# Kernel tuning notes

Hardware: AMD Instinct MI355X
Metric: run time of the kernel (lower is better)

## Reference

```python
import jax, jax.numpy as jnp
import numpy as np

N_NODES = 50000
N_EDGES = 800000
IN_C = 256
HID_C = 256
OUT_C = 128
N_GRAPHS = 256


def setup_inputs() -> dict:
    key = jax.random.key(0)
    ks = jax.random.split(key, 12)
    x = jax.random.normal(ks[0], (N_NODES, IN_C), dtype=jnp.float32)
    src = jax.random.randint(ks[1], (N_EDGES,), 0, N_NODES, dtype=jnp.int32)
    dst = jnp.sort(jax.random.randint(ks[2], (N_EDGES,), 0, N_NODES, dtype=jnp.int32))
    p = jax.random.uniform(ks[3], (N_NODES,), dtype=jnp.float32)
    batch = jnp.sort(jax.random.randint(ks[4], (N_NODES,), 0, N_GRAPHS, dtype=jnp.int32))
    root_ptr = jax.random.randint(ks[5], (N_GRAPHS,), 0, N_NODES, dtype=jnp.int32)
    s1 = 1.0 / np.sqrt(IN_C)
    s2 = 1.0 / np.sqrt(HID_C)
    s3 = 1.0 / np.sqrt(2 * HID_C)
    Wl1 = jax.random.uniform(ks[6], (IN_C, HID_C), jnp.float32, -s1, s1)
    Wr1 = jax.random.uniform(ks[7], (IN_C, HID_C), jnp.float32, -s1, s1)
    b1 = jnp.zeros((HID_C,), jnp.float32)
    Wl2 = jax.random.uniform(ks[8], (HID_C, HID_C), jnp.float32, -s2, s2)
    Wr2 = jax.random.uniform(ks[9], (HID_C, HID_C), jnp.float32, -s2, s2)
    b2 = jnp.zeros((HID_C,), jnp.float32)
    Wlin = jax.random.uniform(ks[10], (2 * HID_C, OUT_C), jnp.float32, -s3, s3)
    blin = jax.random.uniform(ks[11], (OUT_C,), jnp.float32, -s3, s3)
    return {"x": x, "src": src, "dst": dst, "p": p, "batch": batch,
            "root_ptr": root_ptr, "num_graphs": N_GRAPHS,
            "Wl1": Wl1, "Wr1": Wr1, "b1": b1,
            "Wl2": Wl2, "Wr2": Wr2, "b2": b2,
            "Wlin": Wlin, "blin": blin}


def _sage_conv(x, src, dst, inv_deg, Wl, Wr, b):
    # mean aggregation of neighbor features: scatter-add then divide by degree
    agg = jax.ops.segment_sum(x[src], dst, num_segments=N_NODES)  # [N, d]
    agg = agg * inv_deg[:, None]
    return agg @ Wl + x @ Wr + b


def reference(x, src, dst, p, batch, root_ptr, num_graphs,
              Wl1, Wr1, b1, Wl2, Wr2, b2, Wlin, blin):
    # in-degree for mean aggregation (shared by both convs)
    deg = jax.ops.segment_sum(jnp.ones_like(dst, dtype=x.dtype), dst,
                              num_segments=N_NODES)
    inv_deg = jnp.where(deg > 0, 1.0 / jnp.maximum(deg, 1.0), 0.0)

    h = _sage_conv(x, src, dst, inv_deg, Wl1, Wr1, b1)
    h = jax.nn.relu(h)  # dropout is identity in eval mode
    h = _sage_conv(h, src, dst, inv_deg, Wl2, Wr2, b2)

    # masked mean pool of p-weighted features per graph
    pw = h * p[:, None]
    gsum = jax.ops.segment_sum(pw, batch, num_segments=num_graphs)
    gcnt = jax.ops.segment_sum(jnp.ones_like(p), batch, num_segments=num_graphs)
    gmean = gsum / jnp.maximum(gcnt, 1.0)[:, None]

    feat = jnp.concatenate([h[root_ptr], gmean], axis=-1)  # [G, 2*hid]
    return feat @ Wlin + blin
```

## Files before the change

kernel.cpp:

```cpp
#include <hip/hip_runtime.h>
#include <hip/hip_bf16.h>

#define N_NODES 50000
#define N_EDGES 800000
#define C_DIM   256
#define OUT_C   128
#define N_GRAPHS 256

typedef unsigned short ushort8 __attribute__((ext_vector_type(8)));
typedef __bf16         bf16x8  __attribute__((ext_vector_type(8)));
typedef float          f32x4   __attribute__((ext_vector_type(4)));

typedef __attribute__((address_space(1))) const unsigned int gu32;
typedef __attribute__((address_space(3))) unsigned int lu32;

#if __has_builtin(__builtin_amdgcn_sched_barrier)
#define SCHED_FENCE() __builtin_amdgcn_sched_barrier(0)
#else
#define SCHED_FENCE() ((void)0)
#endif

__device__ __forceinline__ float us2f(unsigned short u) {
    unsigned int x = ((unsigned int)u) << 16;
    return __builtin_bit_cast(float, x);
}
__device__ __forceinline__ unsigned short f2bf(float f) {
    unsigned int u = __builtin_bit_cast(unsigned int, f);
    u += 0x7fffu + ((u >> 16) & 1u);
    return (unsigned short)(u >> 16);
}

__device__ __forceinline__ int lower_bound_i(const int* __restrict__ a, int n, int v) {
    int lo = 0, hi = n;
    while (lo < hi) {
        int mid = (lo + hi) >> 1;
        if (a[mid] < v) lo = mid + 1; else hi = mid;
    }
    return lo;
}

__global__ void preprocess(const float* __restrict__ x, unsigned short* __restrict__ xb,
                           const float* __restrict__ W0, const float* __restrict__ W1,
                           const float* __restrict__ W2, const float* __restrict__ W3,
                           unsigned short* __restrict__ D0, unsigned short* __restrict__ D1,
                           unsigned short* __restrict__ D2, unsigned short* __restrict__ D3,
                           const int* __restrict__ dst, const int* __restrict__ batch,
                           int* __restrict__ row_ptr, int* __restrict__ graph_ptr,
                           float* __restrict__ inv_deg) {
    int b = blockIdx.x;
    int t = threadIdx.x;
    if (b < 12500) {
        int i = b * 256 + t;
        float4 v = *(const float4*)(x + ((size_t)i << 2));
        ushort4 o;
        o.x = f2bf(v.x); o.y = f2bf(v.y); o.z = f2bf(v.z); o.w = f2bf(v.w);
        *(ushort4*)(xb + ((size_t)i << 2)) = o;
    } else if (b < 13524) {
        int sub = b - 12500;
        const float* S; unsigned short* D;
        switch (sub >> 8) {
            case 0: S = W0; D = D0; break;
            case 1: S = W1; D = D1; break;
            case 2: S = W2; D = D2; break;
            default: S = W3; D = D3; break;
        }
        int i = (sub & 255) * 256 + t;
        int k = i >> 8, n = i & 255;
        D[n * 256 + k] = f2bf(S[i]);
    } else {
        int i = (b - 13524) * 256 + t;
        if (i <= N_NODES) {
            int lb = lower_bound_i(dst, N_EDGES, i);
            row_ptr[i] = lb;
            if (i < N_NODES) {
                int ub = lower_bound_i(dst, N_EDGES, i + 1);
                int cnt = ub - lb;
                inv_deg[i] = (cnt > 0) ? (1.0f / (float)cnt) : 0.0f;
            }
        }
        if (i <= N_GRAPHS) graph_ptr[i] = lower_bound_i(batch, N_NODES, i);
    }
}

__global__ void aggregate(const unsigned short* __restrict__ X,
                          const int* __restrict__ src,
                          const int* __restrict__ row_ptr,
                          const float* __restrict__ inv_deg,
                          unsigned short* __restrict__ out) {
    int gw   = (blockIdx.x * blockDim.x + threadIdx.x) >> 6;
    int lane = threadIdx.x & 63;
    if (gw >= N_NODES) return;
    int e0 = row_ptr[gw], e1 = row_ptr[gw + 1];
    const int lo = lane << 2;
    float a0 = 0.f, a1 = 0.f, a2 = 0.f, a3 = 0.f;
    int e = e0;

    for (; e + 16 <= e1; e += 16) {
        ushort4 v[16];
#pragma unroll
        for (int j = 0; j < 16; ++j) {
            int s = __builtin_amdgcn_readfirstlane(src[e + j]);
            v[j] = *(const ushort4*)(X + ((size_t)s << 8) + lo);
        }
        SCHED_FENCE();
#pragma unroll
        for (int j = 0; j < 16; ++j) {
            a0 += us2f(v[j].x); a1 += us2f(v[j].y);
            a2 += us2f(v[j].z); a3 += us2f(v[j].w);
        }
    }
    int rem = e1 - e;
    if (rem > 0) {
        int cl = e1 - 1;
        ushort4 v[16]; float w[16];
#pragma unroll
        for (int j = 0; j < 16; ++j) {
            int ej = e + j;
            int ec = ej < cl ? ej : cl;
            w[j] = (ej < e1) ? 1.0f : 0.0f;
            int s = __builtin_amdgcn_readfirstlane(src[ec]);
            v[j] = *(const ushort4*)(X + ((size_t)s << 8) + lo);
        }
        SCHED_FENCE();
#pragma unroll
        for (int j = 0; j < 16; ++j) {
            a0 = fmaf(us2f(v[j].x), w[j], a0);
            a1 = fmaf(us2f(v[j].y), w[j], a1);
            a2 = fmaf(us2f(v[j].z), w[j], a2);
            a3 = fmaf(us2f(v[j].w), w[j], a3);
        }
    }

    float sc = inv_deg[gw];
    ushort4 o;
    o.x = f2bf(a0 * sc); o.y = f2bf(a1 * sc); o.z = f2bf(a2 * sc); o.w = f2bf(a3 * sc);
    *(ushort4*)(out + ((size_t)gw << 8) + lo) = o;
}

__global__ __launch_bounds__(256, 3)
void gemm_fused(const unsigned short* __restrict__ A1,
                const unsigned short* __restrict__ A2,
                const unsigned short* __restrict__ B1t,
                const unsigned short* __restrict__ B2t,
                const float* __restrict__ bias,
                unsigned short* __restrict__ C,
                int M, int do_relu) {
    __shared__ __align__(16) unsigned short As[4096];
    __shared__ __align__(16) unsigned short Bs[16384];

    const int t    = threadIdx.x;
    const int m0   = blockIdx.x * 64;
    const int lane = t & 63, wid = t >> 6;
    const int wn   = wid * 64;
    const int lrow = lane & 15;
    const int kq   = lane >> 4;

    const f32x4 zero4 = {0.f, 0.f, 0.f, 0.f};
    f32x4 acc[4][4];
#pragma unroll
    for (int i = 0; i < 4; ++i)
#pragma unroll
        for (int j = 0; j < 4; ++j) acc[i][j] = zero4;

    for (int it = 0; it < 8; ++it) {
        const unsigned short* __restrict__ Ab = (it < 4) ? A1 : A2;
        const unsigned short* __restrict__ Bb = (it < 4) ? B1t : B2t;
        int ko = (it * 64) & 255;

#pragma unroll
        for (int i = 0; i < 2; ++i) {
            int q   = t + i * 256;
            int row = q >> 3;
            int kb  = (q & 7) ^ (row & 7);
            const unsigned short* ga = Ab + (size_t)(m0 + row) * 256 + ko + kb * 8;
            __builtin_amdgcn_global_load_lds((gu32*)ga, (lu32*)(As + q * 8), 16, 0, 0);
        }
#pragma unroll
        for (int i = 0; i < 8; ++i) {
            int q   = t + i * 256;
            int row = q >> 3;
            int kb  = (q & 7) ^ (row & 7);
            const unsigned short* gb = Bb + (size_t)row * 256 + ko + kb * 8;
            __builtin_amdgcn_global_load_lds((gu32*)gb, (lu32*)(Bs + q * 8), 16, 0, 0);
        }
        __syncthreads();

#pragma unroll
        for (int s = 0; s < 2; ++s) {
            int kqp = s * 4 + kq;
            bf16x8 af[4], bfr[4];
#pragma unroll
            for (int mi = 0; mi < 4; ++mi) {
                int r = mi * 16 + lrow;
                int slot = r * 8 + (kqp ^ (lrow & 7));
                uint4 u = *(const uint4*)(As + slot * 8);
                af[mi] = __builtin_bit_cast(bf16x8, u);
            }
#pragma unroll
            for (int ni = 0; ni < 4; ++ni) {
                int r = wn + ni * 16 + lrow;
                int slot = r * 8 + (kqp ^ (lrow & 7));
                uint4 u = *(const uint4*)(Bs + slot * 8);
                bfr[ni] = __builtin_bit_cast(bf16x8, u);
            }
#pragma unroll
            for (int mi = 0; mi < 4; ++mi)
#pragma unroll
                for (int ni = 0; ni < 4; ++ni)
                    acc[mi][ni] = __builtin_amdgcn_mfma_f32_16x16x32_bf16(
                        af[mi], bfr[ni], acc[mi][ni], 0, 0, 0);
        }
        __syncthreads();
    }

    const int rbase = (lane >> 4) * 4;
#pragma unroll
    for (int ni = 0; ni < 4; ++ni) {
        int n  = wn + ni * 16 + lrow;
        float bv = bias[n];
#pragma unroll
        for (int mi = 0; mi < 4; ++mi) {
            int mb = m0 + mi * 16 + rbase;
#pragma unroll
            for (int r = 0; r < 4; ++r) {
                int m = mb + r;
                if (m < M) {
                    float v = acc[mi][ni][r] + bv;
                    if (do_relu) v = fmaxf(v, 0.f);
                    C[(size_t)m * 256 + n] = f2bf(v);
                }
            }
        }
    }
}

__global__ void pool_final(const unsigned short* __restrict__ h2,
                           const float* __restrict__ p,
                           const int* __restrict__ graph_ptr,
                           const int* __restrict__ root_ptr,
                           const float* __restrict__ Wlin,
                           const float* __restrict__ blin,
                           float* __restrict__ out) {
    __shared__ float fl[512];
    int g = blockIdx.x;
    int c = threadIdx.x;
    int s = graph_ptr[g], e = graph_ptr[g + 1];
    float acc = 0.f;
    for (int n = s; n < e; n += 8) {
        int cl = e - 1;
        float w[8]; unsigned short v[8];
#pragma unroll
        for (int j = 0; j < 8; ++j) {
            int nj = n + j;
            int ncj = nj < cl ? nj : cl;
            int nu = __builtin_amdgcn_readfirstlane(ncj);
            w[j] = (nj < e) ? p[nu] : 0.0f;
            v[j] = h2[(size_t)nu * 256 + c];
        }
        SCHED_FENCE();
#pragma unroll
        for (int j = 0; j < 8; ++j)
            acc = fmaf(us2f(v[j]), w[j], acc);
    }
    float cnt = (float)(e - s);
    int root = root_ptr[g];
    fl[c]       = us2f(h2[(size_t)root * 256 + c]);
    fl[256 + c] = acc / fmaxf(cnt, 1.0f);
    __syncthreads();

    int o = threadIdx.x;
    if (o < 128) {
        float s0 = 0.f, s1 = 0.f, s2 = 0.f, s3 = 0.f;
        for (int k = 0; k < 512; k += 4) {
            s0 = fmaf(fl[k + 0], Wlin[(k + 0) * 128 + o], s0);
            s1 = fmaf(fl[k + 1], Wlin[(k + 1) * 128 + o], s1);
            s2 = fmaf(fl[k + 2], Wlin[(k + 2) * 128 + o], s2);
            s3 = fmaf(fl[k + 3], Wlin[(k + 3) * 128 + o], s3);
        }
        out[(size_t)g * 128 + o] = blin[o] + ((s0 + s1) + (s2 + s3));
    }
}

extern "C" void kernel_launch(void* const* d_in, const int* in_sizes, int n_in,
                              void* d_out, int out_size, void* d_ws, size_t ws_size,
                              hipStream_t stream) {
    const float* x        = (const float*)d_in[0];
    const int*   src      = (const int*)d_in[1];
    const int*   dst      = (const int*)d_in[2];
    const float* p        = (const float*)d_in[3];
    const int*   batch    = (const int*)d_in[4];
    const int*   root_ptr = (const int*)d_in[5];
    const float* Wl1  = (const float*)d_in[7];
    const float* Wr1  = (const float*)d_in[8];
    const float* b1   = (const float*)d_in[9];
    const float* Wl2  = (const float*)d_in[10];
    const float* Wr2  = (const float*)d_in[11];
    const float* b2   = (const float*)d_in[12];
    const float* Wlin = (const float*)d_in[13];
    const float* blin = (const float*)d_in[14];
    float* out = (float*)d_out;

    size_t off = 0;
    char* base = (char*)d_ws;
    auto alloc = [&](size_t bytes) -> void* {
        void* q = base + off;
        off += (bytes + 255) & ~(size_t)255;
        return q;
    };
    int*            row_ptr   = (int*)  alloc((N_NODES + 1) * sizeof(int));
    int*            graph_ptr = (int*)  alloc((N_GRAPHS + 1) * sizeof(int));
    float*          inv_deg   = (float*)alloc(N_NODES * sizeof(float));
    unsigned short* Wl1t = (unsigned short*)alloc(256 * 256 * 2);
    unsigned short* Wr1t = (unsigned short*)alloc(256 * 256 * 2);
    unsigned short* Wl2t = (unsigned short*)alloc(256 * 256 * 2);
    unsigned short* Wr2t = (unsigned short*)alloc(256 * 256 * 2);
    unsigned short* xb   = (unsigned short*)alloc((size_t)N_NODES * 256 * 2);
    unsigned short* aggb = (unsigned short*)alloc((size_t)N_NODES * 256 * 2);
    unsigned short* h1   = (unsigned short*)alloc((size_t)N_NODES * 256 * 2);
    unsigned short* h2   = (unsigned short*)alloc((size_t)N_NODES * 256 * 2);
    (void)ws_size; (void)n_in; (void)in_sizes; (void)out_size;

    preprocess<<<13720, 256, 0, stream>>>(x, xb, Wl1, Wr1, Wl2, Wr2,
                                          Wl1t, Wr1t, Wl2t, Wr2t,
                                          dst, batch, row_ptr, graph_ptr, inv_deg);

    dim3 ggrid((N_NODES + 63) / 64);

    aggregate<<<N_NODES / 4, 256, 0, stream>>>(xb, src, row_ptr, inv_deg, aggb);
    gemm_fused<<<ggrid, 256, 0, stream>>>(aggb, xb, Wl1t, Wr1t, b1, h1, N_NODES, 1);

    aggregate<<<N_NODES / 4, 256, 0, stream>>>(h1, src, row_ptr, inv_deg, aggb);
    gemm_fused<<<ggrid, 256, 0, stream>>>(aggb, h1, Wl2t, Wr2t, b2, h2, N_NODES, 0);

    pool_final<<<N_GRAPHS, 256, 0, stream>>>(h2, p, graph_ptr, root_ptr,
                                             Wlin, blin, out);
}
```

Before: 345.2 us.

## Fuse neighbor aggregation into SAGE conv GEMM via LDS-resident tile

Merges the mean-aggregation gather and the dual GEMM into one kernel per layer: each block gathers 64 rows of neighbor means into a swizzled LDS tile, then runs MFMA against it and the self features. This removes the global write and reread of the aggregated buffer and one launch per layer. B weights and self-features are now read directly from global memory per fragment instead of staged through LDS, and gather parallelism per block is reduced, which risks worse latency hiding.

New measurement: 386.4 us. +11.9%, slower.

```diff
diff --git a/kernel.cpp b/kernel.cpp
--- a/kernel.cpp
+++ b/kernel.cpp
@@ -10,9 +10,6 @@
 typedef unsigned short ushort8 __attribute__((ext_vector_type(8)));
 typedef __bf16         bf16x8  __attribute__((ext_vector_type(8)));
 typedef float          f32x4   __attribute__((ext_vector_type(4)));
-
-typedef __attribute__((address_space(1))) const unsigned int gu32;
-typedef __attribute__((address_space(3))) unsigned int lu32;
 
 #if __has_builtin(__builtin_amdgcn_sched_barrier)
 #define SCHED_FENCE() __builtin_amdgcn_sched_barrier(0)
@@ -82,75 +79,76 @@
     }
 }
 
-__global__ void aggregate(const unsigned short* __restrict__ X,
-                          const int* __restrict__ src,
-                          const int* __restrict__ row_ptr,
-                          const float* __restrict__ inv_deg,
-                          unsigned short* __restrict__ out) {
-    int gw   = (blockIdx.x * blockDim.x + threadIdx.x) >> 6;
-    int lane = threadIdx.x & 63;
-    if (gw >= N_NODES) return;
-    int e0 = row_ptr[gw], e1 = row_ptr[gw + 1];
-    const int lo = lane << 2;
-    float a0 = 0.f, a1 = 0.f, a2 = 0.f, a3 = 0.f;
-    int e = e0;
-
-    for (; e + 16 <= e1; e += 16) {
-        ushort4 v[16];
-#pragma unroll
-        for (int j = 0; j < 16; ++j) {
-            int s = __builtin_amdgcn_readfirstlane(src[e + j]);
-            v[j] = *(const ushort4*)(X + ((size_t)s << 8) + lo);
-        }
-        SCHED_FENCE();
-#pragma unroll
-        for (int j = 0; j < 16; ++j) {
-            a0 += us2f(v[j].x); a1 += us2f(v[j].y);
-            a2 += us2f(v[j].z); a3 += us2f(v[j].w);
-        }
-    }
-    int rem = e1 - e;
-    if (rem > 0) {
-        int cl = e1 - 1;
-        ushort4 v[16]; float w[16];
-#pragma unroll
-        for (int j = 0; j < 16; ++j) {
-            int ej = e + j;
-            int ec = ej < cl ? ej : cl;
-            w[j] = (ej < e1) ? 1.0f : 0.0f;
-            int s = __builtin_amdgcn_readfirstlane(src[ec]);
-            v[j] = *(const ushort4*)(X + ((size_t)s << 8) + lo);
-        }
-        SCHED_FENCE();
-#pragma unroll
-        for (int j = 0; j < 16; ++j) {
-            a0 = fmaf(us2f(v[j].x), w[j], a0);
-            a1 = fmaf(us2f(v[j].y), w[j], a1);
-            a2 = fmaf(us2f(v[j].z), w[j], a2);
-            a3 = fmaf(us2f(v[j].w), w[j], a3);
-        }
-    }
-
-    float sc = inv_deg[gw];
-    ushort4 o;
-    o.x = f2bf(a0 * sc); o.y = f2bf(a1 * sc); o.z = f2bf(a2 * sc); o.w = f2bf(a3 * sc);
-    *(ushort4*)(out + ((size_t)gw << 8) + lo) = o;
-}
-
 __global__ __launch_bounds__(256, 3)
-void gemm_fused(const unsigned short* __restrict__ A1,
-                const unsigned short* __restrict__ A2,
-                const unsigned short* __restrict__ B1t,
-                const unsigned short* __restrict__ B2t,
+void conv_fused(const unsigned short* __restrict__ X,
+                const int* __restrict__ src,
+                const int* __restrict__ row_ptr,
+                const float* __restrict__ inv_deg,
+                const unsigned short* __restrict__ Blt,
+                const unsigned short* __restrict__ Brt,
                 const float* __restrict__ bias,
                 unsigned short* __restrict__ C,
-                int M, int do_relu) {
-    __shared__ __align__(16) unsigned short As[4096];
-    __shared__ __align__(16) unsigned short Bs[16384];
+                int do_relu) {
+    __shared__ __align__(16) unsigned short Agg[16384];
 
     const int t    = threadIdx.x;
     const int m0   = blockIdx.x * 64;
     const int lane = t & 63, wid = t >> 6;
+    const int lo   = lane << 2;
+
+    for (int rr = 0; rr < 16; ++rr) {
+        int r  = wid * 16 + rr;
+        int gw = m0 + r;
+        float a0 = 0.f, a1 = 0.f, a2 = 0.f, a3 = 0.f;
+        float sc = 0.f;
+        if (gw < N_NODES) {
+            int e0 = row_ptr[gw], e1 = row_ptr[gw + 1];
+            sc = inv_deg[gw];
+            int e = e0;
+            for (; e + 16 <= e1; e += 16) {
+                ushort4 v[16];
+#pragma unroll
+                for (int j = 0; j < 16; ++j) {
+                    int s = __builtin_amdgcn_readfirstlane(src[e + j]);
+                    v[j] = *(const ushort4*)(X + ((size_t)s << 8) + lo);
+                }
+                SCHED_FENCE();
+#pragma unroll
+                for (int j = 0; j < 16; ++j) {
+                    a0 += us2f(v[j].x); a1 += us2f(v[j].y);
+                    a2 += us2f(v[j].z); a3 += us2f(v[j].w);
+                }
+            }
+            if (e < e1) {
+                int cl = e1 - 1;
+                ushort4 v[16]; float w[16];
+#pragma unroll
+                for (int j = 0; j < 16; ++j) {
+                    int ej = e + j;
+                    int ec = ej < cl ? ej : cl;
+                    w[j] = (ej < e1) ? 1.0f : 0.0f;
+                    int s = __builtin_amdgcn_readfirstlane(src[ec]);
+                    v[j] = *(const ushort4*)(X + ((size_t)s << 8) + lo);
+                }
+                SCHED_FENCE();
+#pragma unroll
+                for (int j = 0; j < 16; ++j) {
+                    a0 = fmaf(us2f(v[j].x), w[j], a0);
+                    a1 = fmaf(us2f(v[j].y), w[j], a1);
+                    a2 = fmaf(us2f(v[j].z), w[j], a2);
+                    a3 = fmaf(us2f(v[j].w), w[j], a3);
+                }
+            }
+        }
+        ushort4 o;
+        o.x = f2bf(a0 * sc); o.y = f2bf(a1 * sc);
+        o.z = f2bf(a2 * sc); o.w = f2bf(a3 * sc);
+        int c    = lane >> 1;
+        int slot = r * 32 + (c ^ (r & 31));
+        *(ushort4*)(Agg + slot * 8 + (lane & 1) * 4) = o;
+    }
+    __syncthreads();
+
     const int wn   = wid * 64;
     const int lrow = lane & 15;
     const int kq   = lane >> 4;
@@ -163,44 +161,34 @@
         for (int j = 0; j < 4; ++j) acc[i][j] = zero4;
 
     for (int it = 0; it < 8; ++it) {
-        const unsigned short* __restrict__ Ab = (it < 4) ? A1 : A2;
-        const unsigned short* __restrict__ Bb = (it < 4) ? B1t : B2t;
+        const unsigned short* __restrict__ Bb = (it < 4) ? Blt : Brt;
         int ko = (it * 64) & 255;
 
 #pragma unroll
-        for (int i = 0; i < 2; ++i) {
-            int q   = t + i * 256;
-            int row = q >> 3;
-            int kb  = (q & 7) ^ (row & 7);
-            const unsigned short* ga = Ab + (size_t)(m0 + row) * 256 + ko + kb * 8;
-            __builtin_amdgcn_global_load_lds((gu32*)ga, (lu32*)(As + q * 8), 16, 0, 0);
-        }
-#pragma unroll
-        for (int i = 0; i < 8; ++i) {
-            int q   = t + i * 256;
-            int row = q >> 3;
-            int kb  = (q & 7) ^ (row & 7);
-            const unsigned short* gb = Bb + (size_t)row * 256 + ko + kb * 8;
-            __builtin_amdgcn_global_load_lds((gu32*)gb, (lu32*)(Bs + q * 8), 16, 0, 0);
-        }
-        __syncthreads();
-
-#pragma unroll
         for (int s = 0; s < 2; ++s) {
-            int kqp = s * 4 + kq;
+            int kk = ko + s * 32 + kq * 8;
             bf16x8 af[4], bfr[4];
-#pragma unroll
-            for (int mi = 0; mi < 4; ++mi) {
-                int r = mi * 16 + lrow;
-                int slot = r * 8 + (kqp ^ (lrow & 7));
-                uint4 u = *(const uint4*)(As + slot * 8);
-                af[mi] = __builtin_bit_cast(bf16x8, u);
+            if (it < 4) {
+                int c = kk >> 3;
+#pragma unroll
+                for (int mi = 0; mi < 4; ++mi) {
+                    int r = mi * 16 + lrow;
+                    int slot = r * 32 + (c ^ (r & 31));
+                    uint4 u = *(const uint4*)(Agg + slot * 8);
+                    af[mi] = __builtin_bit_cast(bf16x8, u);
+                }
+            } else {
+#pragma unroll
+                for (int mi = 0; mi < 4; ++mi) {
+                    int m = m0 + mi * 16 + lrow;
+                    uint4 u = *(const uint4*)(X + (size_t)m * 256 + kk);
+                    af[mi] = __builtin_bit_cast(bf16x8, u);
+                }
             }
 #pragma unroll
             for (int ni = 0; ni < 4; ++ni) {
-                int r = wn + ni * 16 + lrow;
-                int slot = r * 8 + (kqp ^ (lrow & 7));
-                uint4 u = *(const uint4*)(Bs + slot * 8);
+                int n = wn + ni * 16 + lrow;
+                uint4 u = *(const uint4*)(Bb + (size_t)n * 256 + kk);
                 bfr[ni] = __builtin_bit_cast(bf16x8, u);
             }
 #pragma unroll
@@ -210,7 +198,6 @@
                     acc[mi][ni] = __builtin_amdgcn_mfma_f32_16x16x32_bf16(
                         af[mi], bfr[ni], acc[mi][ni], 0, 0, 0);
         }
-        __syncthreads();
     }
 
     const int rbase = (lane >> 4) * 4;
@@ -224,7 +211,7 @@
 #pragma unroll
             for (int r = 0; r < 4; ++r) {
                 int m = mb + r;
-                if (m < M) {
+                if (m < N_NODES) {
                     float v = acc[mi][ni][r] + bv;
                     if (do_relu) v = fmaxf(v, 0.f);
                     C[(size_t)m * 256 + n] = f2bf(v);
@@ -315,7 +302,6 @@
     unsigned short* Wl2t = (unsigned short*)alloc(256 * 256 * 2);
     unsigned short* Wr2t = (unsigned short*)alloc(256 * 256 * 2);
     unsigned short* xb   = (unsigned short*)alloc((size_t)N_NODES * 256 * 2);
-    unsigned short* aggb = (unsigned short*)alloc((size_t)N_NODES * 256 * 2);
     unsigned short* h1   = (unsigned short*)alloc((size_t)N_NODES * 256 * 2);
     unsigned short* h2   = (unsigned short*)alloc((size_t)N_NODES * 256 * 2);
     (void)ws_size; (void)n_in; (void)in_sizes; (void)out_size;
@@ -324,13 +310,12 @@
                                           Wl1t, Wr1t, Wl2t, Wr2t,
                                           dst, batch, row_ptr, graph_ptr, inv_deg);
 
-    dim3 ggrid((N_NODES + 63) / 64);
-
-    aggregate<<<N_NODES / 4, 256, 0, stream>>>(xb, src, row_ptr, inv_deg, aggb);
-    gemm_fused<<<ggrid, 256, 0, stream>>>(aggb, xb, Wl1t, Wr1t, b1, h1, N_NODES, 1);
-
-    aggregate<<<N_NODES / 4, 256, 0, stream>>>(h1, src, row_ptr, inv_deg, aggb);
-    gemm_fused<<<ggrid, 256, 0, stream>>>(aggb, h1, Wl2t, Wr2t, b2, h2, N_NODES, 0);
+    dim3 cgrid((N_NODES + 63) / 64);
+
+    conv_fused<<<cgrid, 256, 0, stream>>>(xb, src, row_ptr, inv_deg,
+                                          Wl1t, Wr1t, b1, h1, 1);
+    conv_fused<<<cgrid, 256, 0, stream>>>(h1, src, row_ptr, inv_deg,
+                                          Wl2t, Wr2t, b2, h2, 0);
 
     pool_final<<<N_GRAPHS, 256, 0, stream>>>(h2, p, graph_ptr, root_ptr,
                                              Wlin, blin, out);
```
